# Performance work log

Measured on AMD Instinct MI355X. Metric: run time of the kernel, lower is better.

Reference implementation:

```python
import jax, jax.numpy as jnp
import numpy as np

N_EMBD = 1024
N_HEAD = 16
HEAD_SIZE = N_EMBD // N_HEAD  # 64
B, T = 4, 2048

def setup_inputs() -> dict:
    key = jax.random.key(0)
    k1, k2, k3, k4 = jax.random.split(key, 4)
    x = jax.random.normal(k1, (B, T, N_EMBD), dtype=jnp.float32)
    # weights stored as [in, out]; torch Linear does x @ W.T with W [out,in]
    w_qkv = jax.random.normal(k2, (N_EMBD, 3 * N_EMBD), dtype=jnp.float32) * (N_EMBD ** -0.5)
    w_proj = jax.random.normal(k3, (N_EMBD, N_EMBD), dtype=jnp.float32) * (N_EMBD ** -0.5)
    b_proj = jax.random.normal(k4, (N_EMBD,), dtype=jnp.float32) * 0.01
    return {"x": x, "w_qkv": w_qkv, "w_proj": w_proj, "b_proj": b_proj}

def reference(x, w_qkv, w_proj, b_proj):
    Bx, Tx, C = x.shape
    H, D = N_HEAD, HEAD_SIZE
    qkv = x @ w_qkv                               # [B,T,3C]
    q, k, v = jnp.split(qkv, 3, axis=-1)
    q = q.reshape(Bx, Tx, H, D).transpose(0, 2, 1, 3)  # [B,H,T,D]
    k = k.reshape(Bx, Tx, H, D).transpose(0, 2, 1, 3)
    v = v.reshape(Bx, Tx, H, D).transpose(0, 2, 1, 3)
    att = jnp.einsum('bhqd,bhkd->bhqk', q, k) * (D ** -0.5)  # [B,H,T,T]
    causal = jnp.tril(jnp.ones((Tx, Tx), dtype=bool))
    att = jnp.where(causal[None, None], att, -jnp.inf)
    att = jax.nn.softmax(att, axis=-1)
    out = jnp.einsum('bhqk,bhkd->bhqd', att, v)   # [B,H,T,D]
    out = out.transpose(0, 2, 1, 3).reshape(Bx, Tx, H * D)
    return out @ w_proj + b_proj
```

## Files before the change

### kernel.cpp

```cpp
#include <hip/hip_runtime.h>
#include <hip/hip_bf16.h>
#include <stdint.h>
#include <math.h>


typedef __attribute__((ext_vector_type(8))) short short8;
typedef __attribute__((ext_vector_type(4))) float f32x4;

#define LOG2E 1.44269504088896340736f
#define QSCALE 0.18033688011112042f

__device__ int g_isf32;

__device__ __forceinline__ void gl16(const void* g, void* l) {
  __builtin_amdgcn_global_load_lds(
      (const __attribute__((address_space(1))) unsigned int*)g,
      (__attribute__((address_space(3))) unsigned int*)l, 16, 0, 0);
}

__device__ __forceinline__ short f2bf(float f) {
  __hip_bfloat16 h = __float2bfloat16(f);
  return *reinterpret_cast<short*>(&h);
}
__device__ __forceinline__ float bf2f(short s) {
  __hip_bfloat16 h = *reinterpret_cast<__hip_bfloat16*>(&s);
  return __bfloat162float(h);
}
__device__ __forceinline__ short8 pack8(f32x4 lo, f32x4 hi) {
  short8 r;
#pragma unroll
  for (int e = 0; e < 4; ++e) { r[e] = f2bf(lo[e]); r[4 + e] = f2bf(hi[e]); }
  return r;
}

__device__ __forceinline__ short pbf(float f) {
  unsigned u = __builtin_bit_cast(unsigned, f);
  return (short)((u + 0x8000u) >> 16);
}

__device__ __forceinline__ float dpp_max16(float x) {
  int i;
  i = __builtin_amdgcn_update_dpp(0, __builtin_bit_cast(int, x), 0xB1, 0xF, 0xF, true);
  x = fmaxf(x, __builtin_bit_cast(float, i));
  i = __builtin_amdgcn_update_dpp(0, __builtin_bit_cast(int, x), 0x4E, 0xF, 0xF, true);
  x = fmaxf(x, __builtin_bit_cast(float, i));
  i = __builtin_amdgcn_update_dpp(0, __builtin_bit_cast(int, x), 0x141, 0xF, 0xF, true);
  x = fmaxf(x, __builtin_bit_cast(float, i));
  i = __builtin_amdgcn_update_dpp(0, __builtin_bit_cast(int, x), 0x140, 0xF, 0xF, true);
  x = fmaxf(x, __builtin_bit_cast(float, i));
  return x;
}
__device__ __forceinline__ float dpp_sum16(float x) {
  int i;
  i = __builtin_amdgcn_update_dpp(0, __builtin_bit_cast(int, x), 0xB1, 0xF, 0xF, true);
  x += __builtin_bit_cast(float, i);
  i = __builtin_amdgcn_update_dpp(0, __builtin_bit_cast(int, x), 0x4E, 0xF, 0xF, true);
  x += __builtin_bit_cast(float, i);
  i = __builtin_amdgcn_update_dpp(0, __builtin_bit_cast(int, x), 0x141, 0xF, 0xF, true);
  x += __builtin_bit_cast(float, i);
  i = __builtin_amdgcn_update_dpp(0, __builtin_bit_cast(int, x), 0x140, 0xF, 0xF, true);
  x += __builtin_bit_cast(float, i);
  return x;
}

__global__ __launch_bounds__(256) void detect_dtype(const unsigned short* w) {
  __shared__ int cnt;
  if (threadIdx.x == 0) cnt = 0;
  __syncthreads();
  const unsigned short* p = w + (long)blockIdx.x * 49152;
  int c = 0;
  for (int i = threadIdx.x; i < 49152; i += 256)
    if (((p[i] >> 7) & 0xFF) == 0xFF) c++;
  atomicAdd(&cnt, c);
  __syncthreads();
  if (threadIdx.x == 0) g_isf32 = (cnt > 8) ? 1 : 0;
}

__global__ __launch_bounds__(256) void cvt_x(const void* __restrict__ src,
                                             short* __restrict__ dst) {
  const long i = ((long)blockIdx.x * 256 + threadIdx.x) * 8;
  if (g_isf32) {
    const float* s = (const float*)src + i;
    *(short8*)(dst + i) = pack8(*(const f32x4*)s, *(const f32x4*)(s + 4));
  } else {
    *(short8*)(dst + i) = *(const short8*)((const short*)src + i);
  }
}

template <int MODE>
__global__ __launch_bounds__(512, 2) void gemm_bt(
    const short* __restrict__ A, const short* __restrict__ Bt,
    const void* __restrict__ bias, void* __restrict__ C,
    short* __restrict__ vt, int M, int N, int K)
{
  __shared__ __align__(16) short As[3][16384];
  __shared__ __align__(16) short Bs[3][8192];
  const int tid  = threadIdx.x;
  const int lane = tid & 63;
  const int wave = tid >> 6;
  const int quad = lane >> 4;
  const int l16  = lane & 15;
  const int wm = (wave >> 1) * 64;
  const int wn = (wave & 1) * 64;

  const int gx = (int)gridDim.x;
  const int nwg = gx * (int)gridDim.y;
  int lb = (int)blockIdx.y * gx + (int)blockIdx.x;
  if ((nwg & 7) == 0) lb = (lb & 7) * (nwg >> 3) + (lb >> 3);
  const long m0 = (long)(lb / gx) * 256;
  const long n0 = (long)(lb % gx) * 128;

  int isf32 = 0;
  if (MODE == 1) {
    isf32 = g_isf32;
    asm volatile("s_waitcnt vmcnt(0) lgkmcnt(0)" ::: "memory");
  }

  f32x4 acc[4][4] = {};

  const int srow = tid >> 3;
  const int scol = ((tid & 7) ^ (srow & 7)) * 8;
  const short* Ag = A  + (m0 + srow) * (long)K + scol;
  const short* Bg = Bt + (n0 + srow) * (long)K + scol;
  const long rs64 = (long)64 * K;

  const int x7  = l16 & 7;
  const int xo0 = ((0 + quad) ^ x7) * 16;
  const int xo1 = ((4 + quad) ^ x7) * 16;
  const int aRow = (wm + l16) * 128;
  const int bRow = (wn + l16) * 128;

  auto STAGE = [&](int t) {
    const int b = t % 3;
    const long k0 = (long)t << 6;
#pragma unroll
    for (int g = 0; g < 4; ++g)
      gl16(Ag + k0 + g * rs64, (char*)As[b] + g * 8192 + tid * 16);
#pragma unroll
    for (int g = 0; g < 2; ++g)
      gl16(Bg + k0 + g * rs64, (char*)Bs[b] + g * 8192 + tid * 16);
  };

  const int nt = K >> 6;
  STAGE(0);
  STAGE(1);

  for (int t = 0; t < nt; ++t) {
    if (t + 1 < nt) { asm volatile("s_waitcnt vmcnt(6)" ::: "memory"); }
    else            { asm volatile("s_waitcnt vmcnt(0)" ::: "memory"); }
    __builtin_amdgcn_sched_barrier(0);
    __builtin_amdgcn_s_barrier();
    if (t + 2 < nt) STAGE(t + 2);

    const char* Ab = (const char*)As[t % 3];
    const char* Bb = (const char*)Bs[t % 3];
    short8 af[4][2], bfv[4][2];
#pragma unroll
    for (int i = 0; i < 4; ++i) {
      af[i][0] = *(const short8*)(Ab + aRow + i * 2048 + xo0);
      af[i][1] = *(const short8*)(Ab + aRow + i * 2048 + xo1);
    }
#pragma unroll
    for (int j = 0; j < 4; ++j) {
      bfv[j][0] = *(const short8*)(Bb + bRow + j * 2048 + xo0);
      bfv[j][1] = *(const short8*)(Bb + bRow + j * 2048 + xo1);
    }
    __builtin_amdgcn_s_setprio(1);
#pragma unroll
    for (int i = 0; i < 4; ++i)
#pragma unroll
      for (int j = 0; j < 4; ++j) {
        acc[i][j] = __builtin_amdgcn_mfma_f32_16x16x32_bf16(af[i][0], bfv[j][0], acc[i][j], 0, 0, 0);
        acc[i][j] = __builtin_amdgcn_mfma_f32_16x16x32_bf16(af[i][1], bfv[j][1], acc[i][j], 0, 0, 0);
      }
    __builtin_amdgcn_s_setprio(0);
  }

#pragma unroll
  for (int j = 0; j < 4; ++j) {
    const long col = n0 + wn + j * 16 + l16;
    float bv = 0.f;
    if (MODE == 1)
      bv = isf32 ? ((const float*)bias)[col] : bf2f(((const short*)bias)[col]);
#pragma unroll
    for (int i = 0; i < 4; ++i) {
      const long row0 = m0 + wm + i * 16 + quad * 4;
#pragma unroll
      for (int r = 0; r < 4; ++r) {
        const long row = row0 + r;
        const float val = acc[i][j][r] + bv;
        if (MODE == 2) {
          if (col < 2048) {
            const float vq = (col < 1024) ? val * QSCALE : val;
            ((short*)C)[row * 2048 + col] = f2bf(vq);
          } else {
            const long b = row >> 11, t = row & 2047;
            const long hd = col - 2048;
            vt[((b * 16 + (hd >> 6)) * 64 + (hd & 63)) * 2048 + t] = f2bf(val);
          }
        } else {
          if (isf32) ((float*)C)[row * (long)N + col] = val;
          else       ((short*)C)[row * (long)N + col] = f2bf(val);
        }
      }
    }
  }
}

__global__ __launch_bounds__(256) void transpose64(
    const void* __restrict__ src, short* __restrict__ dst, int R, int C)
{
  __shared__ __align__(16) short tile[64][72];
  const int isf32 = g_isf32;
  const int tid = threadIdx.x;
  const long r0 = (long)blockIdx.y * 64;
  const long c0 = (long)blockIdx.x * 64;
#pragma unroll
  for (int it = 0; it < 2; ++it) {
    int idx = it * 256 + tid;
    int rr = idx >> 3, ch = idx & 7;
    const long off = (r0 + rr) * C + c0 + ch * 8;
    short8 v;
    if (isf32) {
      const float* s = (const float*)src + off;
      v = pack8(*(const f32x4*)s, *(const f32x4*)(s + 4));
    } else {
      v = *(const short8*)((const short*)src + off);
    }
    *(short8*)&tile[rr][ch * 8] = v;
  }
  __syncthreads();
#pragma unroll
  for (int it = 0; it < 2; ++it) {
    int idx = it * 256 + tid;
    int cc = idx >> 3, ch = idx & 7;
    short8 v;
#pragma unroll
    for (int jj = 0; jj < 8; ++jj) v[jj] = tile[ch * 8 + jj][cc];
    *(short8*)&dst[(c0 + cc) * R + r0 + ch * 8] = v;
  }
}

__global__ __launch_bounds__(256) void attn_fwd(
    const short* __restrict__ qk, const short* __restrict__ vt,
    short* __restrict__ out)
{
  __shared__ __align__(16) short Ks[2][64][32];
  __shared__ __align__(16) short Vs[2][64][32];
  __shared__ __align__(16) short Pw[4][16][76];
  const int tid = threadIdx.x;
  const int lane = tid & 63, wave = tid >> 6;
  const int quad = lane >> 4, l16 = lane & 15;
  const int bh = blockIdx.x;
  const int b = bh >> 4, h = bh & 15;
  const int jq = (int)gridDim.y - 1 - (int)blockIdx.y;
  const int qbase = jq * 64 + wave * 16;

  const short* qp = qk + ((long)(b * 2048 + qbase + l16)) * 2048 + h * 64 + quad * 8;
  const short8 aq0 = *(const short8*)qp;
  const short8 aq1 = *(const short8*)(qp + 32);

  const int sr = tid >> 2, sc_ = tid & 3;
  const short* kg = qk + (long)b * 2048 * 2048 + 1024 + h * 64 + (long)sr * 2048 + sc_ * 8;
  const short* vg = vt + ((long)bh * 64 + sr) * 2048 + sc_ * 8;

  f32x4 o[4] = {};
  float m_run[4], l_run[4];
#pragma unroll
  for (int r = 0; r < 4; ++r) { m_run[r] = -1e30f; l_run[r] = 0.f; }

  for (int kt = 0; kt < jq; ++kt) {
    const int k0 = kt * 64;

    __syncthreads();
    gl16(kg + (long)k0 * 2048,      (char*)Ks + tid * 16);
    gl16(kg + (long)k0 * 2048 + 32, (char*)Ks + 4096 + tid * 16);
    gl16(vg + k0,                   (char*)Vs + tid * 16);
    gl16(vg + k0 + 32,              (char*)Vs + 4096 + tid * 16);
    __syncthreads();

    f32x4 s[4];
#pragma unroll
    for (int c = 0; c < 4; ++c) {
      short8 kf0 = *(const short8*)&Ks[0][c * 16 + l16][quad * 8];
      short8 kf1 = *(const short8*)&Ks[1][c * 16 + l16][quad * 8];
      f32x4 z = {};
      z = __builtin_amdgcn_mfma_f32_16x16x32_bf16(aq0, kf0, z, 0, 0, 0);
      z = __builtin_amdgcn_mfma_f32_16x16x32_bf16(aq1, kf1, z, 0, 0, 0);
      s[c] = z;
    }

    float mx[4];
#pragma unroll
    for (int r = 0; r < 4; ++r)
      mx[r] = dpp_max16(fmaxf(fmaxf(s[0][r], s[1][r]), fmaxf(s[2][r], s[3][r])));

    int grow = 0;
#pragma unroll
    for (int r = 0; r < 4; ++r) grow |= (mx[r] > m_run[r] + 8.f);
    if (__any(grow)) {
#pragma unroll
      for (int r = 0; r < 4; ++r) {
        const float mn = fmaxf(m_run[r], mx[r]);
        const float al = __builtin_amdgcn_exp2f(m_run[r] - mn);
        m_run[r] = mn;
        l_run[r] *= al;
#pragma unroll
        for (int i = 0; i < 4; ++i) o[i][r] *= al;
      }
    }

#pragma unroll
    for (int c = 0; c < 4; ++c)
#pragma unroll
      for (int r = 0; r < 4; ++r) {
        const float p = __builtin_amdgcn_exp2f(s[c][r] - m_run[r]);
        l_run[r] += p;
        Pw[wave][quad * 4 + r][c * 16 + l16] = pbf(p);
      }

    {
      short8 pf0 = *(const short8*)&Pw[wave][l16][quad * 8];
      short8 pf1 = *(const short8*)&Pw[wave][l16][32 + quad * 8];
#pragma unroll
      for (int i = 0; i < 4; ++i) {
        short8 vf0 = *(const short8*)&Vs[0][i * 16 + l16][quad * 8];
        o[i] = __builtin_amdgcn_mfma_f32_16x16x32_bf16(pf0, vf0, o[i], 0, 0, 0);
        short8 vf1 = *(const short8*)&Vs[1][i * 16 + l16][quad * 8];
        o[i] = __builtin_amdgcn_mfma_f32_16x16x32_bf16(pf1, vf1, o[i], 0, 0, 0);
      }
    }
  }

  {
    const int k0 = jq * 64;

    __syncthreads();
    gl16(kg + (long)k0 * 2048,      (char*)Ks + tid * 16);
    gl16(kg + (long)k0 * 2048 + 32, (char*)Ks + 4096 + tid * 16);
    gl16(vg + k0,                   (char*)Vs + tid * 16);
    gl16(vg + k0 + 32,              (char*)Vs + 4096 + tid * 16);
    __syncthreads();

    f32x4 s[4];
    float mx[4];
#pragma unroll
    for (int r = 0; r < 4; ++r) mx[r] = -1e30f;
#pragma unroll
    for (int c = 0; c < 4; ++c) {
      if (c > wave) continue;
      short8 kf0 = *(const short8*)&Ks[0][c * 16 + l16][quad * 8];
      short8 kf1 = *(const short8*)&Ks[1][c * 16 + l16][quad * 8];
      f32x4 z = {};
      z = __builtin_amdgcn_mfma_f32_16x16x32_bf16(aq0, kf0, z, 0, 0, 0);
      z = __builtin_amdgcn_mfma_f32_16x16x32_bf16(aq1, kf1, z, 0, 0, 0);
      if (c == wave) {
#pragma unroll
        for (int r = 0; r < 4; ++r)
          z[r] = (l16 > quad * 4 + r) ? -1e30f : z[r];
      }
      s[c] = z;
#pragma unroll
      for (int r = 0; r < 4; ++r) mx[r] = fmaxf(mx[r], z[r]);
    }
#pragma unroll
    for (int r = 0; r < 4; ++r) mx[r] = dpp_max16(mx[r]);

    int grow = 0;
#pragma unroll
    for (int r = 0; r < 4; ++r) grow |= (mx[r] > m_run[r] + 8.f);
    if (__any(grow)) {
#pragma unroll
      for (int r = 0; r < 4; ++r) {
        const float mn = fmaxf(m_run[r], mx[r]);
        const float al = __builtin_amdgcn_exp2f(m_run[r] - mn);
        m_run[r] = mn;
        l_run[r] *= al;
#pragma unroll
        for (int i = 0; i < 4; ++i) o[i][r] *= al;
      }
    }

#pragma unroll
    for (int c = 0; c < 4; ++c) {
      if (c <= wave) {
#pragma unroll
        for (int r = 0; r < 4; ++r) {
          const float p = __builtin_amdgcn_exp2f(s[c][r] - m_run[r]);
          l_run[r] += p;
          Pw[wave][quad * 4 + r][c * 16 + l16] = pbf(p);
        }
      } else if (c < 2 || wave >= 2) {
#pragma unroll
        for (int r = 0; r < 4; ++r)
          Pw[wave][quad * 4 + r][c * 16 + l16] = 0;
      }
    }

    {
      short8 pf0 = *(const short8*)&Pw[wave][l16][quad * 8];
#pragma unroll
      for (int i = 0; i < 4; ++i) {
        short8 vf0 = *(const short8*)&Vs[0][i * 16 + l16][quad * 8];
        o[i] = __builtin_amdgcn_mfma_f32_16x16x32_bf16(pf0, vf0, o[i], 0, 0, 0);
      }
      if (wave >= 2) {
        short8 pf1 = *(const short8*)&Pw[wave][l16][32 + quad * 8];
#pragma unroll
        for (int i = 0; i < 4; ++i) {
          short8 vf1 = *(const short8*)&Vs[1][i * 16 + l16][quad * 8];
          o[i] = __builtin_amdgcn_mfma_f32_16x16x32_bf16(pf1, vf1, o[i], 0, 0, 0);
        }
      }
    }
  }

#pragma unroll
  for (int r = 0; r < 4; ++r) l_run[r] = dpp_sum16(l_run[r]);
  float inv[4];
#pragma unroll
  for (int r = 0; r < 4; ++r) inv[r] = 1.0f / l_run[r];
  short* op = out + ((long)(b * 2048 + qbase + quad * 4)) * 1024 + h * 64;
#pragma unroll
  for (int i = 0; i < 4; ++i)
#pragma unroll
    for (int r = 0; r < 4; ++r)
      op[(long)r * 1024 + i * 16 + l16] = f2bf(o[i][r] * inv[r]);
}

__global__ __launch_bounds__(256) void copy_out(const void* __restrict__ src,
                                                void* __restrict__ dst)
{
  const long n16 = g_isf32 ? 2097152L : 1048576L;
  const uint4* s = (const uint4*)src;
  uint4* d = (uint4*)dst;
  for (long i = (long)blockIdx.x * 256 + threadIdx.x; i < n16;
       i += (long)gridDim.x * 256)
    d[i] = s[i];
}

extern "C" void kernel_launch(void* const* d_in, const int* in_sizes, int n_in,
                              void* d_out, int out_size, void* d_ws, size_t ws_size,
                              hipStream_t stream)
{
  const void* x      = d_in[0];
  const void* w_qkv  = d_in[1];
  const void* w_proj = d_in[2];
  const void* b_proj = d_in[3];

  short* ws = (short*)d_ws;
  const bool planA = ws_size >= 67108864ULL;

  short* qk  = ws;
  short* vtp = ws + 16777216L;

  short *wqkvT, *attnb, *wprojT, *xbf;
  void*  projC;
  if (planA) {
    attnb  = ws + 25165824L;
    wqkvT  = attnb;
    wprojT = qk;
    xbf    = (short*)d_out;
    projC  = d_out;
  } else {
    wqkvT  = (short*)d_out;
    xbf    = (short*)d_out + 3145728L;
    attnb  = (short*)d_out;
    wprojT = vtp;
    projC  = qk;
  }

  detect_dtype<<<64, 256, 0, stream>>>((const unsigned short*)w_qkv);
  cvt_x<<<4096, 256, 0, stream>>>(x, xbf);
  transpose64<<<dim3(3072 / 64, 1024 / 64), 256, 0, stream>>>(w_qkv, wqkvT, 1024, 3072);
  gemm_bt<2><<<dim3(3072 / 128, 8192 / 256), 512, 0, stream>>>(
      xbf, wqkvT, nullptr, qk, vtp, 8192, 3072, 1024);
  attn_fwd<<<dim3(64, 32), 256, 0, stream>>>(qk, vtp, attnb);
  transpose64<<<dim3(1024 / 64, 1024 / 64), 256, 0, stream>>>(w_proj, wprojT, 1024, 1024);
  gemm_bt<1><<<dim3(1024 / 128, 8192 / 256), 512, 0, stream>>>(
      attnb, wprojT, b_proj, projC, nullptr, 8192, 1024, 1024);
  if (!planA)
    copy_out<<<2048, 256, 0, stream>>>(projC, d_out);
}
```

Measured before the change: 321.2 us.

## Split GEMM K-tile into two phases interleaving LDS loads, prefetch, and MFMA

The GEMM main loop now processes each 64-wide K tile in two halves. Each half loads its A/B fragments from LDS, issues half of the next-next tile's global-to-LDS prefetch, then runs its MFMAs, with an extra barrier between halves. The V-transpose epilogue also writes four consecutive time rows as one 8-byte vector store instead of four scalar stores. This aims to spread global loads across compute, cut register pressure from fragments, and make the V store coalesced, at the cost of an extra barrier per tile.

```diff
diff --git a/kernel.cpp b/kernel.cpp
--- a/kernel.cpp
+++ b/kernel.cpp
@@ -5,6 +5,7 @@
 
 
 typedef __attribute__((ext_vector_type(8))) short short8;
+typedef __attribute__((ext_vector_type(4))) short shrt4;
 typedef __attribute__((ext_vector_type(4))) float f32x4;
 
 #define LOG2E 1.44269504088896340736f
@@ -130,50 +131,51 @@
   const int aRow = (wm + l16) * 128;
   const int bRow = (wn + l16) * 128;
 
-  auto STAGE = [&](int t) {
-    const int b = t % 3;
-    const long k0 = (long)t << 6;
-#pragma unroll
-    for (int g = 0; g < 4; ++g)
-      gl16(Ag + k0 + g * rs64, (char*)As[b] + g * 8192 + tid * 16);
-#pragma unroll
-    for (int g = 0; g < 2; ++g)
-      gl16(Bg + k0 + g * rs64, (char*)Bs[b] + g * 8192 + tid * 16);
+  auto STAGE_HALF = [&](int t2, int h) {
+    const int bb = t2 % 3;
+    const long k0 = (long)t2 << 6;
+    gl16(Ag + k0 + (h * 2 + 0) * rs64, (char*)As[bb] + (h * 2 + 0) * 8192 + tid * 16);
+    gl16(Ag + k0 + (h * 2 + 1) * rs64, (char*)As[bb] + (h * 2 + 1) * 8192 + tid * 16);
+    gl16(Bg + k0 + h * rs64,           (char*)Bs[bb] + h * 8192 + tid * 16);
   };
 
   const int nt = K >> 6;
-  STAGE(0);
-  STAGE(1);
+  STAGE_HALF(0, 0); STAGE_HALF(0, 1);
+  STAGE_HALF(1, 0); STAGE_HALF(1, 1);
 
   for (int t = 0; t < nt; ++t) {
     if (t + 1 < nt) { asm volatile("s_waitcnt vmcnt(6)" ::: "memory"); }
     else            { asm volatile("s_waitcnt vmcnt(0)" ::: "memory"); }
     __builtin_amdgcn_sched_barrier(0);
     __builtin_amdgcn_s_barrier();
-    if (t + 2 < nt) STAGE(t + 2);
+    __builtin_amdgcn_sched_barrier(0);
 
     const char* Ab = (const char*)As[t % 3];
     const char* Bb = (const char*)Bs[t % 3];
-    short8 af[4][2], bfv[4][2];
-#pragma unroll
-    for (int i = 0; i < 4; ++i) {
-      af[i][0] = *(const short8*)(Ab + aRow + i * 2048 + xo0);
-      af[i][1] = *(const short8*)(Ab + aRow + i * 2048 + xo1);
-    }
-#pragma unroll
-    for (int j = 0; j < 4; ++j) {
-      bfv[j][0] = *(const short8*)(Bb + bRow + j * 2048 + xo0);
-      bfv[j][1] = *(const short8*)(Bb + bRow + j * 2048 + xo1);
-    }
-    __builtin_amdgcn_s_setprio(1);
-#pragma unroll
-    for (int i = 0; i < 4; ++i)
-#pragma unroll
-      for (int j = 0; j < 4; ++j) {
-        acc[i][j] = __builtin_amdgcn_mfma_f32_16x16x32_bf16(af[i][0], bfv[j][0], acc[i][j], 0, 0, 0);
-        acc[i][j] = __builtin_amdgcn_mfma_f32_16x16x32_bf16(af[i][1], bfv[j][1], acc[i][j], 0, 0, 0);
-      }
-    __builtin_amdgcn_s_setprio(0);
+
+#pragma unroll
+    for (int ph = 0; ph < 2; ++ph) {
+      const int xo = ph ? xo1 : xo0;
+      short8 af[4], bfv[4];
+#pragma unroll
+      for (int i = 0; i < 4; ++i)
+        af[i] = *(const short8*)(Ab + aRow + i * 2048 + xo);
+#pragma unroll
+      for (int j = 0; j < 4; ++j)
+        bfv[j] = *(const short8*)(Bb + bRow + j * 2048 + xo);
+      if (t + 2 < nt) STAGE_HALF(t + 2, ph);
+      __builtin_amdgcn_s_setprio(1);
+#pragma unroll
+      for (int i = 0; i < 4; ++i)
+#pragma unroll
+        for (int j = 0; j < 4; ++j)
+          acc[i][j] = __builtin_amdgcn_mfma_f32_16x16x32_bf16(af[i], bfv[j], acc[i][j], 0, 0, 0);
+      __builtin_amdgcn_s_setprio(0);
+      if (ph == 0) {
+        __builtin_amdgcn_s_barrier();
+        __builtin_amdgcn_sched_barrier(0);
+      }
+    }
   }
 
 #pragma unroll
@@ -185,22 +187,25 @@
 #pragma unroll
     for (int i = 0; i < 4; ++i) {
       const long row0 = m0 + wm + i * 16 + quad * 4;
-#pragma unroll
-      for (int r = 0; r < 4; ++r) {
-        const long row = row0 + r;
-        const float val = acc[i][j][r] + bv;
-        if (MODE == 2) {
-          if (col < 2048) {
+      if (MODE == 2 && col >= 2048) {
+        const long bb = row0 >> 11, t0 = row0 & 2047;
+        const long hd = col - 2048;
+        shrt4 v4;
+#pragma unroll
+        for (int r = 0; r < 4; ++r) v4[r] = f2bf(acc[i][j][r]);
+        *(shrt4*)&vt[((bb * 16 + (hd >> 6)) * 64 + (hd & 63)) * 2048 + t0] = v4;
+      } else {
+#pragma unroll
+        for (int r = 0; r < 4; ++r) {
+          const long row = row0 + r;
+          const float val = acc[i][j][r] + bv;
+          if (MODE == 2) {
             const float vq = (col < 1024) ? val * QSCALE : val;
             ((short*)C)[row * 2048 + col] = f2bf(vq);
           } else {
-            const long b = row >> 11, t = row & 2047;
-            const long hd = col - 2048;
-            vt[((b * 16 + (hd >> 6)) * 64 + (hd & 63)) * 2048 + t] = f2bf(val);
+            if (isf32) ((float*)C)[row * (long)N + col] = val;
+            else       ((short*)C)[row * (long)N + col] = f2bf(val);
           }
-        } else {
-          if (isf32) ((float*)C)[row * (long)N + col] = val;
-          else       ((short*)C)[row * (long)N + col] = f2bf(val);
         }
       }
     }
```

Result: faster. 286.4 us (-10.8%).
